# Kernel tuning notes

Measured on AMD Instinct MI355X. Metric: run time of the kernel, lower is better.

The kernel has to match this reference:

```python
import jax, jax.numpy as jnp
import numpy as np

N = 50000        # nodes
E = 800000       # edges (before self-loops)
IN = 512         # in_channels
HEADS = 8        # 'head' arg: heads and per-head out dim of conv1
C1 = 8           # per-head channels of conv1 (== head)
OUT = 128        # out_channels of conv2
NEG_SLOPE = 0.2  # PyG GATConv leaky-relu slope


def _glorot(key, shape, fan_in):
    return jax.random.normal(key, shape, jnp.float32) * (1.0 / np.sqrt(fan_in))


def setup_inputs() -> dict:
    key = jax.random.key(0)
    ks = jax.random.split(key, 10)
    x = jax.random.normal(ks[0], (N, IN), jnp.float32)
    edge_index = jax.random.randint(ks[1], (2, E), 0, N, dtype=jnp.int32)
    # conv1: GATConv(IN, C1, heads=HEADS, concat=True)
    W1 = _glorot(ks[2], (IN, HEADS * C1), IN)
    att_src1 = _glorot(ks[3], (HEADS, C1), C1)
    att_dst1 = _glorot(ks[4], (HEADS, C1), C1)
    bias1 = jnp.zeros((HEADS * C1,), jnp.float32)
    # conv2: GATConv(HEADS*C1, OUT, heads=1, concat=False)
    W2 = _glorot(ks[5], (HEADS * C1, OUT), HEADS * C1)
    att_src2 = _glorot(ks[6], (1, OUT), OUT)
    att_dst2 = _glorot(ks[7], (1, OUT), OUT)
    bias2 = jnp.zeros((OUT,), jnp.float32)
    return {"x": x, "edge_index": edge_index,
            "W1": W1, "att_src1": att_src1, "att_dst1": att_dst1, "bias1": bias1,
            "W2": W2, "att_src2": att_src2, "att_dst2": att_dst2, "bias2": bias2}


def gat_conv(x, src, dst, W, a_src, a_dst, bias, heads, concat):
    """PyG GATConv (eval mode, dropout off). src/dst already include self-loops."""
    n = x.shape[0]
    h = (x @ W).reshape(n, heads, -1)                 # [N, H, C]
    s = (h * a_src[None]).sum(-1)                     # [N, H] alpha_src per node
    d = (h * a_dst[None]).sum(-1)                     # [N, H] alpha_dst per node
    alpha = jax.nn.leaky_relu(s[src] + d[dst], NEG_SLOPE)  # [E, H]
    # segment softmax over incoming edges of each destination node
    amax = jax.ops.segment_max(alpha, dst, num_segments=n)  # [N, H]
    amax = jnp.where(jnp.isfinite(amax), amax, 0.0)
    ea = jnp.exp(alpha - amax[dst])                   # [E, H]
    denom = jax.ops.segment_sum(ea, dst, num_segments=n)
    w = ea / (denom[dst] + 1e-16)                     # [E, H]
    msg = h[src] * w[..., None]                       # [E, H, C]
    out = jax.ops.segment_sum(msg, dst, num_segments=n)  # [N, H, C]
    out = out.reshape(n, -1) if concat else out.mean(axis=1)
    return out + bias


def reference(x, edge_index, W1, att_src1, att_dst1, bias1,
              W2, att_src2, att_dst2, bias2):
    n = x.shape[0]
    loop = jnp.arange(n, dtype=edge_index.dtype)      # PyG adds self-loops
    src = jnp.concatenate([edge_index[0], loop])
    dst = jnp.concatenate([edge_index[1], loop])
    h = jax.nn.elu(gat_conv(x, src, dst, W1, att_src1, att_dst1, bias1,
                            heads=HEADS, concat=True))
    out = jax.nn.elu(gat_conv(h, src, dst, W2, att_src2, att_dst2, bias2,
                              heads=1, concat=False))
    return out
```

## Files before the change

### kernel.cpp

```cpp
#include <hip/hip_runtime.h>

#define NEG_SLOPE 0.2f

typedef __attribute__((ext_vector_type(8))) short bf16x8;
typedef __attribute__((ext_vector_type(4))) float f32x4;

__device__ __forceinline__ float leaky(float v) {
    return v > 0.0f ? v : NEG_SLOPE * v;
}
__device__ __forceinline__ float elu(float v) {
    return v > 0.0f ? v : (__expf(v) - 1.0f);
}
__device__ __forceinline__ short f2b(float f) {
    return (short)((__float_as_uint(f) + 0x8000u) >> 16);
}
__device__ __forceinline__ float bf2f(unsigned short v) {
    return __uint_as_float(((unsigned)v) << 16);
}

__global__ void prep_k(const float* __restrict__ W1, const float* __restrict__ W2,
                       unsigned short* __restrict__ w1s, unsigned short* __restrict__ w2s,
                       int* __restrict__ deg, int N) {
    int i = blockIdx.x * 256 + threadIdx.x;
    if (i < N) deg[i] = 0;
    if (i < 512 * 64) {
        int k = i >> 6, n = i & 63;
        int kt = k >> 5, kk = k & 31;
        int nt = n >> 4, nn = n & 15;
        int lane = (kk >> 3) * 16 + nn, j = kk & 7;
        w1s[(((size_t)(kt * 4 + nt)) * 64 + lane) * 8 + j] = (unsigned short)f2b(W1[i]);
    } else if (i < 512 * 64 + 64 * 128) {
        int i2 = i - 512 * 64;
        int k = i2 >> 7, n = i2 & 127;
        int kt = k >> 5, kk = k & 31;
        int nt = n >> 4, nn = n & 15;
        int lane = (kk >> 3) * 16 + nn, j = kk & 7;
        w2s[(((size_t)(kt * 8 + nt)) * 64 + lane) * 8 + j] = (unsigned short)f2b(W2[i2]);
    }
}

__global__ __launch_bounds__(256) void gemm1_k(const float* __restrict__ X,
                                               const unsigned short* __restrict__ Ws,
                                               const float* __restrict__ Asrc,
                                               const float* __restrict__ Adst,
                                               unsigned short* __restrict__ Hb,
                                               float* __restrict__ S,
                                               float* __restrict__ D, int N) {
    const int lane = threadIdx.x & 63;
    const int wave = threadIdx.x >> 6;
    const int m0 = blockIdx.x * 64 + wave * 16;
    const int q = lane >> 4, lc = lane & 15;
    const int arow = m0 + lc;
    const float* xrow = X + (size_t)min(arow, N - 1) * 512 + q * 8;
    const bf16x8* bW = (const bf16x8*)Ws;

    f32x4 acc[4] = {{0.f,0.f,0.f,0.f},{0.f,0.f,0.f,0.f},{0.f,0.f,0.f,0.f},{0.f,0.f,0.f,0.f}};

    for (int kt = 0; kt < 16; ++kt) {
        float4 a0 = *(const float4*)(xrow + kt * 32);
        float4 a1 = *(const float4*)(xrow + kt * 32 + 4);
        bf16x8 af;
        af[0] = f2b(a0.x); af[1] = f2b(a0.y); af[2] = f2b(a0.z); af[3] = f2b(a0.w);
        af[4] = f2b(a1.x); af[5] = f2b(a1.y); af[6] = f2b(a1.z); af[7] = f2b(a1.w);
#pragma unroll
        for (int nt = 0; nt < 4; ++nt) {
            bf16x8 bf = bW[(size_t)(kt * 4 + nt) * 64 + lane];
            acc[nt] = __builtin_amdgcn_mfma_f32_16x16x32_bf16(af, bf, acc[nt], 0, 0, 0);
        }
    }

    float asc[4], adc[4];
#pragma unroll
    for (int nt = 0; nt < 4; ++nt) { asc[nt] = Asrc[nt * 16 + lc]; adc[nt] = Adst[nt * 16 + lc]; }

#pragma unroll
    for (int r = 0; r < 4; ++r) {
        int row = m0 + q * 4 + r;
        bool ok = row < N;
        if (ok) {
#pragma unroll
            for (int nt = 0; nt < 4; ++nt)
                Hb[(size_t)row * 64 + nt * 16 + lc] = (unsigned short)f2b(acc[nt][r]);
        }
        float ps[4], pd[4];
#pragma unroll
        for (int nt = 0; nt < 4; ++nt) { ps[nt] = acc[nt][r] * asc[nt]; pd[nt] = acc[nt][r] * adc[nt]; }
#pragma unroll
        for (int off = 1; off < 8; off <<= 1) {
#pragma unroll
            for (int nt = 0; nt < 4; ++nt) {
                ps[nt] += __shfl_xor(ps[nt], off);
                pd[nt] += __shfl_xor(pd[nt], off);
            }
        }
        if (ok && !(lc & 7)) {
            int hb = lc >> 3;
#pragma unroll
            for (int nt = 0; nt < 4; ++nt) {
                S[(size_t)row * 8 + nt * 2 + hb] = ps[nt];
                D[(size_t)row * 8 + nt * 2 + hb] = pd[nt];
            }
        }
    }
}

__global__ __launch_bounds__(256) void gemm2_k(const unsigned short* __restrict__ X,
                                               const unsigned short* __restrict__ Ws,
                                               const float* __restrict__ Asrc,
                                               const float* __restrict__ Adst,
                                               unsigned short* __restrict__ Hb,
                                               float* __restrict__ S,
                                               float* __restrict__ D, int N) {
    const int lane = threadIdx.x & 63;
    const int wave = threadIdx.x >> 6;
    const int m0 = blockIdx.x * 64 + wave * 16;
    const int q = lane >> 4, lc = lane & 15;
    const int arow = m0 + lc;
    const unsigned short* xrow = X + (size_t)min(arow, N - 1) * 64 + q * 8;
    const bf16x8* bW = (const bf16x8*)Ws;

    f32x4 acc[8] = {{0.f,0.f,0.f,0.f},{0.f,0.f,0.f,0.f},{0.f,0.f,0.f,0.f},{0.f,0.f,0.f,0.f},
                    {0.f,0.f,0.f,0.f},{0.f,0.f,0.f,0.f},{0.f,0.f,0.f,0.f},{0.f,0.f,0.f,0.f}};

#pragma unroll
    for (int kt = 0; kt < 2; ++kt) {
        bf16x8 af = *(const bf16x8*)(xrow + kt * 32);
#pragma unroll
        for (int nt = 0; nt < 8; ++nt) {
            bf16x8 bf = bW[(size_t)(kt * 8 + nt) * 64 + lane];
            acc[nt] = __builtin_amdgcn_mfma_f32_16x16x32_bf16(af, bf, acc[nt], 0, 0, 0);
        }
    }

    float asc[8], adc[8];
#pragma unroll
    for (int nt = 0; nt < 8; ++nt) { asc[nt] = Asrc[nt * 16 + lc]; adc[nt] = Adst[nt * 16 + lc]; }

#pragma unroll
    for (int r = 0; r < 4; ++r) {
        int row = m0 + q * 4 + r;
        bool ok = row < N;
        if (ok) {
#pragma unroll
            for (int nt = 0; nt < 8; ++nt)
                Hb[(size_t)row * 128 + nt * 16 + lc] = (unsigned short)f2b(acc[nt][r]);
        }
        float ps = 0.f, pd = 0.f;
#pragma unroll
        for (int nt = 0; nt < 8; ++nt) { ps += acc[nt][r] * asc[nt]; pd += acc[nt][r] * adc[nt]; }
#pragma unroll
        for (int off = 1; off < 16; off <<= 1) {
            ps += __shfl_xor(ps, off);
            pd += __shfl_xor(pd, off);
        }
        if (ok && lc == 0) { S[row] = ps; D[row] = pd; }
    }
}

__global__ void deg_k(const int* __restrict__ dst, int E, int* __restrict__ deg) {
    int base = (blockIdx.x * blockDim.x + threadIdx.x) * 8;
    if (base + 8 <= E) {
        int4 a = *(const int4*)(dst + base);
        int4 b = *(const int4*)(dst + base + 4);
        atomicAdd(&deg[a.x], 1); atomicAdd(&deg[a.y], 1);
        atomicAdd(&deg[a.z], 1); atomicAdd(&deg[a.w], 1);
        atomicAdd(&deg[b.x], 1); atomicAdd(&deg[b.y], 1);
        atomicAdd(&deg[b.z], 1); atomicAdd(&deg[b.w], 1);
    } else {
        for (int e = base; e < E; ++e) atomicAdd(&deg[dst[e]], 1);
    }
}

__global__ __launch_bounds__(256) void scanA_k(const int* __restrict__ deg,
                                               int* __restrict__ rowptr,
                                               int* __restrict__ partials, int N) {
    __shared__ int s[256];
    const int t = threadIdx.x;
    const int base = blockIdx.x * 1024;
    int v[4];
    int idx = base + t * 4;
#pragma unroll
    for (int i = 0; i < 4; ++i) v[i] = (idx + i < N) ? deg[idx + i] + 1 : 0;
    int sum = v[0] + v[1] + v[2] + v[3];
    s[t] = sum;
    __syncthreads();
    for (int off = 1; off < 256; off <<= 1) {
        int x = (t >= off) ? s[t - off] : 0;
        __syncthreads();
        s[t] += x;
        __syncthreads();
    }
    int run = s[t] - sum;
#pragma unroll
    for (int i = 0; i < 4; ++i) {
        if (idx + i < N) rowptr[idx + i] = run;
        run += v[i];
    }
    if (t == 255) partials[blockIdx.x] = s[255];
}

__global__ __launch_bounds__(256) void scanB_k(const int* __restrict__ partials,
                                               int* __restrict__ poff,
                                               int* __restrict__ rowptr, int nb,
                                               int N, int Etot) {
    __shared__ int s[256];
    const int t = threadIdx.x;
    int v = (t < nb) ? partials[t] : 0;
    s[t] = v;
    __syncthreads();
    for (int off = 1; off < 256; off <<= 1) {
        int x = (t >= off) ? s[t - off] : 0;
        __syncthreads();
        s[t] += x;
        __syncthreads();
    }
    poff[t] = s[t] - v;
    if (t == 0) rowptr[N] = Etot;
}

__global__ void scanC_k(int* __restrict__ rowptr, const int* __restrict__ poff,
                        int* __restrict__ wp, int* __restrict__ srcs, int N) {
    int i = blockIdx.x * blockDim.x + threadIdx.x;
    if (i >= N) return;
    int r = rowptr[i] + poff[i >> 10];
    rowptr[i] = r;
    srcs[r] = i;
    wp[i] = r + 1;
}

__global__ void scatter_k(const int* __restrict__ ei, int E,
                          int* __restrict__ wp, int* __restrict__ srcs) {
    int base = (blockIdx.x * blockDim.x + threadIdx.x) * 4;
    if (base + 4 <= E) {
        int4 s = *(const int4*)(ei + base);
        int4 d = *(const int4*)(ei + E + base);
        int p0 = atomicAdd(&wp[d.x], 1);
        int p1 = atomicAdd(&wp[d.y], 1);
        int p2 = atomicAdd(&wp[d.z], 1);
        int p3 = atomicAdd(&wp[d.w], 1);
        srcs[p0] = s.x; srcs[p1] = s.y; srcs[p2] = s.z; srcs[p3] = s.w;
    } else {
        for (int e = base; e < E; ++e) {
            int p = atomicAdd(&wp[ei[E + e]], 1);
            srcs[p] = ei[e];
        }
    }
}

__global__ __launch_bounds__(256) void agg1_csr_k(const int* __restrict__ rowptr,
                                                  const int* __restrict__ srcs,
                                                  const float* __restrict__ S,
                                                  const float* __restrict__ D,
                                                  const unsigned short* __restrict__ Hb,
                                                  const float* __restrict__ bias,
                                                  unsigned short* __restrict__ out, int N) {
    const int wid = (blockIdx.x * 256 + threadIdx.x) >> 6;
    const int lane = threadIdx.x & 63;
    if (wid >= N) return;
    const int beg = rowptr[wid], end = rowptr[wid + 1];
    const int h = lane & 7;
    const int el = lane >> 3;
    const float dvh = D[(size_t)wid * 8 + h];

    float m = -1e30f;
    for (int i = beg + el; i < end; i += 8)
        m = fmaxf(m, leaky(S[(size_t)srcs[i] * 8 + h] + dvh));
#pragma unroll
    for (int off = 8; off < 64; off <<= 1)
        m = fmaxf(m, __shfl_xor(m, off));

    float acc = 0.0f, den = 0.0f;
    for (int base = beg; base < end; base += 8) {
        int i = base + el;
        int src_l = 0; float w_l = 0.0f;
        if (i < end) {
            src_l = srcs[i];
            w_l = __expf(leaky(S[(size_t)src_l * 8 + h] + dvh) - m);
        }
        den += w_l;
#pragma unroll
        for (int j = 0; j < 8; ++j) {
            float w = __shfl(w_l, j * 8 + (lane >> 3));
            int src = __builtin_amdgcn_readfirstlane(__shfl(src_l, j * 8));
            acc += w * bf2f(Hb[(size_t)src * 64 + lane]);
        }
    }
#pragma unroll
    for (int off = 8; off < 64; off <<= 1)
        den += __shfl_xor(den, off);
    float rden = 1.0f / (__shfl(den, lane >> 3) + 1e-16f);
    out[(size_t)wid * 64 + lane] = (unsigned short)f2b(elu(acc * rden + bias[lane]));
}

__global__ __launch_bounds__(256) void agg2_csr_k(const int* __restrict__ rowptr,
                                                  const int* __restrict__ srcs,
                                                  const float* __restrict__ S,
                                                  const float* __restrict__ D,
                                                  const unsigned short* __restrict__ Hb,
                                                  const float* __restrict__ bias,
                                                  float* __restrict__ out, int N) {
    const int wid = (blockIdx.x * 256 + threadIdx.x) >> 6;
    const int lane = threadIdx.x & 63;
    if (wid >= N) return;
    const int beg = rowptr[wid], end = rowptr[wid + 1];
    const float dvh = D[wid];
    const int c0 = lane * 2;

    float m = -1e30f;
    for (int i = beg + lane; i < end; i += 64)
        m = fmaxf(m, leaky(S[srcs[i]] + dvh));
#pragma unroll
    for (int off = 1; off < 64; off <<= 1)
        m = fmaxf(m, __shfl_xor(m, off));

    float acc0 = 0.0f, acc1 = 0.0f, den = 0.0f;
    for (int base = beg; base < end; base += 64) {
        int i = base + lane;
        int src_l = 0; float w_l = 0.0f;
        if (i < end) {
            src_l = srcs[i];
            w_l = __expf(leaky(S[src_l] + dvh) - m);
        }
        den += w_l;
        const int cnt = min(64, end - base);
        for (int j0 = 0; j0 < cnt; j0 += 8) {
#pragma unroll
            for (int u = 0; u < 8; ++u) {
                int j = j0 + u;
                float w = __shfl(w_l, j);
                int src = __builtin_amdgcn_readfirstlane(__shfl(src_l, j));
                unsigned p = *(const unsigned*)(Hb + (size_t)src * 128 + c0);
                acc0 += w * __uint_as_float(p << 16);
                acc1 += w * __uint_as_float(p & 0xffff0000u);
            }
        }
    }
#pragma unroll
    for (int off = 1; off < 64; off <<= 1)
        den += __shfl_xor(den, off);
    const float rden = 1.0f / (den + 1e-16f);
    float2 o;
    o.x = elu(acc0 * rden + bias[c0]);
    o.y = elu(acc1 * rden + bias[c0 + 1]);
    *(float2*)(out + (size_t)wid * 128 + c0) = o;
}

extern "C" void kernel_launch(void* const* d_in, const int* in_sizes, int n_in,
                              void* d_out, int out_size, void* d_ws, size_t ws_size,
                              hipStream_t stream) {
    const float* x   = (const float*)d_in[0];
    const int*   ei  = (const int*)d_in[1];
    const float* W1  = (const float*)d_in[2];
    const float* as1 = (const float*)d_in[3];
    const float* ad1 = (const float*)d_in[4];
    const float* b1  = (const float*)d_in[5];
    const float* W2  = (const float*)d_in[6];
    const float* as2 = (const float*)d_in[7];
    const float* ad2 = (const float*)d_in[8];
    const float* b2  = (const float*)d_in[9];

    const int N = in_sizes[0] / 512;
    const int E = in_sizes[1] / 2;
    const int Etot = E + N;
    float* out = (float*)d_out;

    unsigned short* w1s    = (unsigned short*)d_ws;
    unsigned short* w2s    = w1s + 512 * 64;
    unsigned short* out1b  = w2s + 64 * 128;
    unsigned short* h1b    = out1b + (size_t)N * 64;
    float*          s1     = (float*)(h1b + (size_t)N * 64);
    float*          d1     = s1 + (size_t)N * 8;
    unsigned short* h2b    = (unsigned short*)(d1 + (size_t)N * 8);
    float*          s2     = (float*)(h2b + (size_t)N * 128);
    float*          d2     = s2 + N;
    int*            rowptr = (int*)(d2 + N);
    int*            srcs   = rowptr + (N + 1);
    int* deg      = (int*)h2b;
    int* wp       = deg + N;
    int* partials = wp + N;
    int* poff     = partials + 256;

    const int B = 256;
    const int nb = (N + 1023) / 1024;
    const int gblk = (N + 63) / 64;
    const int prep_n = (N > 512 * 64 + 64 * 128) ? N : (512 * 64 + 64 * 128);

    prep_k<<<(prep_n + B - 1) / B, B, 0, stream>>>(W1, W2, w1s, w2s, deg, N);
    deg_k<<<(E + B * 8 - 1) / (B * 8), B, 0, stream>>>(ei + E, E, deg);
    scanA_k<<<nb, B, 0, stream>>>(deg, rowptr, partials, N);
    scanB_k<<<1, B, 0, stream>>>(partials, poff, rowptr, nb, N, Etot);
    scanC_k<<<(N + B - 1) / B, B, 0, stream>>>(rowptr, poff, wp, srcs, N);
    scatter_k<<<(E + B * 4 - 1) / (B * 4), B, 0, stream>>>(ei, E, wp, srcs);

    gemm1_k<<<gblk, B, 0, stream>>>(x, w1s, as1, ad1, h1b, s1, d1, N);
    agg1_csr_k<<<(N + 3) / 4, B, 0, stream>>>(rowptr, srcs, s1, d1, h1b, b1, out1b, N);

    gemm2_k<<<gblk, B, 0, stream>>>(out1b, w2s, as2, ad2, h2b, s2, d2, N);
    agg2_csr_k<<<(N + 3) / 4, B, 0, stream>>>(rowptr, srcs, s2, d2, h2b, b2, out, N);
}
```

Measured before the change: 364.8 us.

## Fuse degree count into GEMM1, single-pass ticket scan, fuse agg1 with GEMM2

Degree counting moves into extra blocks of the first GEMM launch, so the GEMM and the atomics run together in one kernel. The three-kernel scan becomes one kernel that takes each chunk's base offset from an atomic ticket counter, and row ends are rebuilt from beg+deg+1 instead of rowptr. The layer-1 aggregation now writes its bf16 results to shared memory and runs the second GEMM there, so out1b no longer goes through global memory. This removes several launches and one round trip through global memory. In exchange, ticket-ordered chunk bases make the CSR layout depend on block scheduling order, and agg1 waves now stall at a block barrier.

```diff
diff --git a/kernel.cpp b/kernel.cpp
--- a/kernel.cpp
+++ b/kernel.cpp
@@ -22,7 +22,7 @@
                        unsigned short* __restrict__ w1s, unsigned short* __restrict__ w2s,
                        int* __restrict__ deg, int N) {
     int i = blockIdx.x * 256 + threadIdx.x;
-    if (i < N) deg[i] = 0;
+    if (i <= N) deg[i] = 0;
     if (i < 512 * 64) {
         int k = i >> 6, n = i & 63;
         int kt = k >> 5, kk = k & 31;
@@ -39,13 +39,31 @@
     }
 }
 
-__global__ __launch_bounds__(256) void gemm1_k(const float* __restrict__ X,
+__global__ __launch_bounds__(256) void g1deg_k(const float* __restrict__ X,
                                                const unsigned short* __restrict__ Ws,
                                                const float* __restrict__ Asrc,
                                                const float* __restrict__ Adst,
                                                unsigned short* __restrict__ Hb,
                                                float* __restrict__ S,
-                                               float* __restrict__ D, int N) {
+                                               float* __restrict__ D,
+                                               const int* __restrict__ dst,
+                                               int* __restrict__ deg,
+                                               int N, int E, int gblk) {
+    if ((int)blockIdx.x >= gblk) {
+        int wtid = ((int)blockIdx.x - gblk) * 256 + threadIdx.x;
+        int base = wtid * 8;
+        if (base + 8 <= E) {
+            int4 a = *(const int4*)(dst + base);
+            int4 b = *(const int4*)(dst + base + 4);
+            atomicAdd(&deg[a.x], 1); atomicAdd(&deg[a.y], 1);
+            atomicAdd(&deg[a.z], 1); atomicAdd(&deg[a.w], 1);
+            atomicAdd(&deg[b.x], 1); atomicAdd(&deg[b.y], 1);
+            atomicAdd(&deg[b.z], 1); atomicAdd(&deg[b.w], 1);
+        } else {
+            for (int e = base; e < E; ++e) atomicAdd(&deg[dst[e]], 1);
+        }
+        return;
+    }
     const int lane = threadIdx.x & 63;
     const int wave = threadIdx.x >> 6;
     const int m0 = blockIdx.x * 64 + wave * 16;
@@ -104,128 +122,39 @@
     }
 }
 
-__global__ __launch_bounds__(256) void gemm2_k(const unsigned short* __restrict__ X,
-                                               const unsigned short* __restrict__ Ws,
-                                               const float* __restrict__ Asrc,
-                                               const float* __restrict__ Adst,
-                                               unsigned short* __restrict__ Hb,
-                                               float* __restrict__ S,
-                                               float* __restrict__ D, int N) {
-    const int lane = threadIdx.x & 63;
-    const int wave = threadIdx.x >> 6;
-    const int m0 = blockIdx.x * 64 + wave * 16;
-    const int q = lane >> 4, lc = lane & 15;
-    const int arow = m0 + lc;
-    const unsigned short* xrow = X + (size_t)min(arow, N - 1) * 64 + q * 8;
-    const bf16x8* bW = (const bf16x8*)Ws;
-
-    f32x4 acc[8] = {{0.f,0.f,0.f,0.f},{0.f,0.f,0.f,0.f},{0.f,0.f,0.f,0.f},{0.f,0.f,0.f,0.f},
-                    {0.f,0.f,0.f,0.f},{0.f,0.f,0.f,0.f},{0.f,0.f,0.f,0.f},{0.f,0.f,0.f,0.f}};
-
-#pragma unroll
-    for (int kt = 0; kt < 2; ++kt) {
-        bf16x8 af = *(const bf16x8*)(xrow + kt * 32);
-#pragma unroll
-        for (int nt = 0; nt < 8; ++nt) {
-            bf16x8 bf = bW[(size_t)(kt * 8 + nt) * 64 + lane];
-            acc[nt] = __builtin_amdgcn_mfma_f32_16x16x32_bf16(af, bf, acc[nt], 0, 0, 0);
-        }
-    }
-
-    float asc[8], adc[8];
-#pragma unroll
-    for (int nt = 0; nt < 8; ++nt) { asc[nt] = Asrc[nt * 16 + lc]; adc[nt] = Adst[nt * 16 + lc]; }
-
-#pragma unroll
-    for (int r = 0; r < 4; ++r) {
-        int row = m0 + q * 4 + r;
-        bool ok = row < N;
-        if (ok) {
-#pragma unroll
-            for (int nt = 0; nt < 8; ++nt)
-                Hb[(size_t)row * 128 + nt * 16 + lc] = (unsigned short)f2b(acc[nt][r]);
-        }
-        float ps = 0.f, pd = 0.f;
-#pragma unroll
-        for (int nt = 0; nt < 8; ++nt) { ps += acc[nt][r] * asc[nt]; pd += acc[nt][r] * adc[nt]; }
-#pragma unroll
-        for (int off = 1; off < 16; off <<= 1) {
-            ps += __shfl_xor(ps, off);
-            pd += __shfl_xor(pd, off);
-        }
-        if (ok && lc == 0) { S[row] = ps; D[row] = pd; }
-    }
-}
-
-__global__ void deg_k(const int* __restrict__ dst, int E, int* __restrict__ deg) {
-    int base = (blockIdx.x * blockDim.x + threadIdx.x) * 8;
-    if (base + 8 <= E) {
-        int4 a = *(const int4*)(dst + base);
-        int4 b = *(const int4*)(dst + base + 4);
-        atomicAdd(&deg[a.x], 1); atomicAdd(&deg[a.y], 1);
-        atomicAdd(&deg[a.z], 1); atomicAdd(&deg[a.w], 1);
-        atomicAdd(&deg[b.x], 1); atomicAdd(&deg[b.y], 1);
-        atomicAdd(&deg[b.z], 1); atomicAdd(&deg[b.w], 1);
-    } else {
-        for (int e = base; e < E; ++e) atomicAdd(&deg[dst[e]], 1);
-    }
-}
-
-__global__ __launch_bounds__(256) void scanA_k(const int* __restrict__ deg,
-                                               int* __restrict__ rowptr,
-                                               int* __restrict__ partials, int N) {
-    __shared__ int s[256];
+__global__ __launch_bounds__(256) void scan_k(const int* __restrict__ deg_in,
+                                              int* __restrict__ ticket,
+                                              int* __restrict__ beg,
+                                              int* __restrict__ wp,
+                                              int* __restrict__ srcs, int N) {
+    __shared__ int sm[256];
+    __shared__ int chunkBase;
     const int t = threadIdx.x;
-    const int base = blockIdx.x * 1024;
+    int idx = blockIdx.x * 1024 + t * 4;
     int v[4];
-    int idx = base + t * 4;
-#pragma unroll
-    for (int i = 0; i < 4; ++i) v[i] = (idx + i < N) ? deg[idx + i] + 1 : 0;
+#pragma unroll
+    for (int i = 0; i < 4; ++i) v[i] = (idx + i < N) ? deg_in[idx + i] + 1 : 0;
     int sum = v[0] + v[1] + v[2] + v[3];
-    s[t] = sum;
+    sm[t] = sum;
     __syncthreads();
     for (int off = 1; off < 256; off <<= 1) {
-        int x = (t >= off) ? s[t - off] : 0;
+        int xv = (t >= off) ? sm[t - off] : 0;
         __syncthreads();
-        s[t] += x;
+        sm[t] += xv;
         __syncthreads();
     }
-    int run = s[t] - sum;
+    if (t == 255) chunkBase = atomicAdd(ticket, sm[255]);
+    __syncthreads();
+    int run = chunkBase + sm[t] - sum;
 #pragma unroll
     for (int i = 0; i < 4; ++i) {
-        if (idx + i < N) rowptr[idx + i] = run;
-        run += v[i];
-    }
-    if (t == 255) partials[blockIdx.x] = s[255];
-}
-
-__global__ __launch_bounds__(256) void scanB_k(const int* __restrict__ partials,
-                                               int* __restrict__ poff,
-                                               int* __restrict__ rowptr, int nb,
-                                               int N, int Etot) {
-    __shared__ int s[256];
-    const int t = threadIdx.x;
-    int v = (t < nb) ? partials[t] : 0;
-    s[t] = v;
-    __syncthreads();
-    for (int off = 1; off < 256; off <<= 1) {
-        int x = (t >= off) ? s[t - off] : 0;
-        __syncthreads();
-        s[t] += x;
-        __syncthreads();
-    }
-    poff[t] = s[t] - v;
-    if (t == 0) rowptr[N] = Etot;
-}
-
-__global__ void scanC_k(int* __restrict__ rowptr, const int* __restrict__ poff,
-                        int* __restrict__ wp, int* __restrict__ srcs, int N) {
-    int i = blockIdx.x * blockDim.x + threadIdx.x;
-    if (i >= N) return;
-    int r = rowptr[i] + poff[i >> 10];
-    rowptr[i] = r;
-    srcs[r] = i;
-    wp[i] = r + 1;
+        if (idx + i < N) {
+            beg[idx + i] = run;
+            srcs[run] = idx + i;
+            wp[idx + i] = run + 1;
+            run += v[i];
+        }
+    }
 }
 
 __global__ void scatter_k(const int* __restrict__ ei, int E,
@@ -247,52 +176,124 @@
     }
 }
 
-__global__ __launch_bounds__(256) void agg1_csr_k(const int* __restrict__ rowptr,
-                                                  const int* __restrict__ srcs,
-                                                  const float* __restrict__ S,
-                                                  const float* __restrict__ D,
-                                                  const unsigned short* __restrict__ Hb,
-                                                  const float* __restrict__ bias,
-                                                  unsigned short* __restrict__ out, int N) {
-    const int wid = (blockIdx.x * 256 + threadIdx.x) >> 6;
-    const int lane = threadIdx.x & 63;
-    if (wid >= N) return;
-    const int beg = rowptr[wid], end = rowptr[wid + 1];
+__global__ __launch_bounds__(256) void agg1g2_k(const int* __restrict__ beg,
+                                                const int* __restrict__ deg,
+                                                const int* __restrict__ srcs,
+                                                const float* __restrict__ S1,
+                                                const float* __restrict__ D1,
+                                                const unsigned short* __restrict__ H1b,
+                                                const float* __restrict__ b1,
+                                                const unsigned short* __restrict__ W2s,
+                                                const float* __restrict__ as2,
+                                                const float* __restrict__ ad2,
+                                                unsigned short* __restrict__ H2b,
+                                                float* __restrict__ S2,
+                                                float* __restrict__ D2, int N) {
+    __shared__ unsigned short sh[16][64];
+    __shared__ float shp[4][16], shq[4][16];
+
+    const int tid  = threadIdx.x;
+    const int lane = tid & 63;
+    const int wave = tid >> 6;
+    const int m0 = blockIdx.x * 16;
+
     const int h = lane & 7;
     const int el = lane >> 3;
-    const float dvh = D[(size_t)wid * 8 + h];
-
-    float m = -1e30f;
-    for (int i = beg + el; i < end; i += 8)
-        m = fmaxf(m, leaky(S[(size_t)srcs[i] * 8 + h] + dvh));
-#pragma unroll
-    for (int off = 8; off < 64; off <<= 1)
-        m = fmaxf(m, __shfl_xor(m, off));
-
-    float acc = 0.0f, den = 0.0f;
-    for (int base = beg; base < end; base += 8) {
-        int i = base + el;
-        int src_l = 0; float w_l = 0.0f;
-        if (i < end) {
-            src_l = srcs[i];
-            w_l = __expf(leaky(S[(size_t)src_l * 8 + h] + dvh) - m);
-        }
-        den += w_l;
-#pragma unroll
-        for (int j = 0; j < 8; ++j) {
-            float w = __shfl(w_l, j * 8 + (lane >> 3));
-            int src = __builtin_amdgcn_readfirstlane(__shfl(src_l, j * 8));
-            acc += w * bf2f(Hb[(size_t)src * 64 + lane]);
-        }
-    }
-#pragma unroll
-    for (int off = 8; off < 64; off <<= 1)
-        den += __shfl_xor(den, off);
-    float rden = 1.0f / (__shfl(den, lane >> 3) + 1e-16f);
-    out[(size_t)wid * 64 + lane] = (unsigned short)f2b(elu(acc * rden + bias[lane]));
-}
-
-__global__ __launch_bounds__(256) void agg2_csr_k(const int* __restrict__ rowptr,
+#pragma unroll
+    for (int rep = 0; rep < 4; ++rep) {
+        const int nl = wave * 4 + rep;
+        const int wid = m0 + nl;
+        if (wid < N) {
+            const int b0 = beg[wid];
+            const int e0 = b0 + deg[wid] + 1;
+            const float dvh = D1[(size_t)wid * 8 + h];
+
+            float m = -1e30f;
+            for (int i = b0 + el; i < e0; i += 8)
+                m = fmaxf(m, leaky(S1[(size_t)srcs[i] * 8 + h] + dvh));
+#pragma unroll
+            for (int off = 8; off < 64; off <<= 1)
+                m = fmaxf(m, __shfl_xor(m, off));
+
+            float acc = 0.0f, den = 0.0f;
+            for (int base = b0; base < e0; base += 8) {
+                int i = base + el;
+                int src_l = 0; float w_l = 0.0f;
+                if (i < e0) {
+                    src_l = srcs[i];
+                    w_l = __expf(leaky(S1[(size_t)src_l * 8 + h] + dvh) - m);
+                }
+                den += w_l;
+#pragma unroll
+                for (int j = 0; j < 8; ++j) {
+                    float w = __shfl(w_l, j * 8 + (lane >> 3));
+                    int src = __builtin_amdgcn_readfirstlane(__shfl(src_l, j * 8));
+                    acc += w * bf2f(H1b[(size_t)src * 64 + lane]);
+                }
+            }
+#pragma unroll
+            for (int off = 8; off < 64; off <<= 1)
+                den += __shfl_xor(den, off);
+            float rden = 1.0f / (__shfl(den, lane >> 3) + 1e-16f);
+            sh[nl][lane] = (unsigned short)f2b(elu(acc * rden + b1[lane]));
+        } else {
+            sh[nl][lane] = 0;
+        }
+    }
+    __syncthreads();
+
+    const int q = lane >> 4, lc = lane & 15;
+    const bf16x8* bW = (const bf16x8*)W2s;
+    const int nt0 = wave * 2;
+
+    f32x4 acc2[2] = {{0.f,0.f,0.f,0.f},{0.f,0.f,0.f,0.f}};
+#pragma unroll
+    for (int kt = 0; kt < 2; ++kt) {
+        bf16x8 af = *(const bf16x8*)(&sh[lc][q * 8 + kt * 32]);
+#pragma unroll
+        for (int u = 0; u < 2; ++u) {
+            bf16x8 bf = bW[(size_t)(kt * 8 + nt0 + u) * 64 + lane];
+            acc2[u] = __builtin_amdgcn_mfma_f32_16x16x32_bf16(af, bf, acc2[u], 0, 0, 0);
+        }
+    }
+    float asc[2], adc[2];
+#pragma unroll
+    for (int u = 0; u < 2; ++u) {
+        asc[u] = as2[(nt0 + u) * 16 + lc];
+        adc[u] = ad2[(nt0 + u) * 16 + lc];
+    }
+#pragma unroll
+    for (int r = 0; r < 4; ++r) {
+        int rl = q * 4 + r;
+        int row = m0 + rl;
+        if (row < N) {
+#pragma unroll
+            for (int u = 0; u < 2; ++u)
+                H2b[(size_t)row * 128 + (nt0 + u) * 16 + lc] = (unsigned short)f2b(acc2[u][r]);
+        }
+        float ps = acc2[0][r] * asc[0] + acc2[1][r] * asc[1];
+        float pd = acc2[0][r] * adc[0] + acc2[1][r] * adc[1];
+#pragma unroll
+        for (int off = 1; off < 16; off <<= 1) {
+            ps += __shfl_xor(ps, off);
+            pd += __shfl_xor(pd, off);
+        }
+        if (lc == 0) { shp[wave][rl] = ps; shq[wave][rl] = pd; }
+    }
+    __syncthreads();
+    if (tid < 16) {
+        int row = m0 + tid;
+        if (row < N) {
+            float s = shp[0][tid] + shp[1][tid] + shp[2][tid] + shp[3][tid];
+            float d = shq[0][tid] + shq[1][tid] + shq[2][tid] + shq[3][tid];
+            S2[row] = s;
+            D2[row] = d;
+        }
+    }
+}
+
+__global__ __launch_bounds__(256) void agg2_csr_k(const int* __restrict__ beg,
+                                                  const int* __restrict__ deg,
                                                   const int* __restrict__ srcs,
                                                   const float* __restrict__ S,
                                                   const float* __restrict__ D,
@@ -302,36 +303,37 @@
     const int wid = (blockIdx.x * 256 + threadIdx.x) >> 6;
     const int lane = threadIdx.x & 63;
     if (wid >= N) return;
-    const int beg = rowptr[wid], end = rowptr[wid + 1];
-    const float dvh = D[wid];
+    const int b0 = beg[wid];
+    const int e0 = b0 + deg[wid] + 1;
+    const float dv = D[wid];
     const int c0 = lane * 2;
 
     float m = -1e30f;
-    for (int i = beg + lane; i < end; i += 64)
-        m = fmaxf(m, leaky(S[srcs[i]] + dvh));
+    for (int i = b0 + lane; i < e0; i += 64)
+        m = fmaxf(m, leaky(S[srcs[i]] + dv));
 #pragma unroll
     for (int off = 1; off < 64; off <<= 1)
         m = fmaxf(m, __shfl_xor(m, off));
 
     float acc0 = 0.0f, acc1 = 0.0f, den = 0.0f;
-    for (int base = beg; base < end; base += 64) {
+    for (int base = b0; base < e0; base += 64) {
         int i = base + lane;
         int src_l = 0; float w_l = 0.0f;
-        if (i < end) {
+        if (i < e0) {
             src_l = srcs[i];
-            w_l = __expf(leaky(S[src_l] + dvh) - m);
+            w_l = __expf(leaky(S[src_l] + dv) - m);
         }
         den += w_l;
-        const int cnt = min(64, end - base);
+        const int cnt = min(64, e0 - base);
         for (int j0 = 0; j0 < cnt; j0 += 8) {
 #pragma unroll
             for (int u = 0; u < 8; ++u) {
                 int j = j0 + u;
                 float w = __shfl(w_l, j);
                 int src = __builtin_amdgcn_readfirstlane(__shfl(src_l, j));
-                unsigned p = *(const unsigned*)(Hb + (size_t)src * 128 + c0);
-                acc0 += w * __uint_as_float(p << 16);
-                acc1 += w * __uint_as_float(p & 0xffff0000u);
+                unsigned pv = *(const unsigned*)(Hb + (size_t)src * 128 + c0);
+                acc0 += w * __uint_as_float(pv << 16);
+                acc1 += w * __uint_as_float(pv & 0xffff0000u);
             }
         }
     }
@@ -361,40 +363,34 @@
 
     const int N = in_sizes[0] / 512;
     const int E = in_sizes[1] / 2;
-    const int Etot = E + N;
-    float* out = (float*)d_out;
-
-    unsigned short* w1s    = (unsigned short*)d_ws;
-    unsigned short* w2s    = w1s + 512 * 64;
-    unsigned short* out1b  = w2s + 64 * 128;
-    unsigned short* h1b    = out1b + (size_t)N * 64;
-    float*          s1     = (float*)(h1b + (size_t)N * 64);
-    float*          d1     = s1 + (size_t)N * 8;
-    unsigned short* h2b    = (unsigned short*)(d1 + (size_t)N * 8);
-    float*          s2     = (float*)(h2b + (size_t)N * 128);
-    float*          d2     = s2 + N;
-    int*            rowptr = (int*)(d2 + N);
-    int*            srcs   = rowptr + (N + 1);
-    int* deg      = (int*)h2b;
-    int* wp       = deg + N;
-    int* partials = wp + N;
-    int* poff     = partials + 256;
+
+    unsigned short* w1s  = (unsigned short*)d_ws;
+    unsigned short* w2s  = w1s + 512 * 64;
+    unsigned short* h1b  = w2s + 64 * 128;
+    unsigned short* h2b  = h1b + (size_t)N * 64;
+    float*          s1   = (float*)(h2b + (size_t)N * 128);
+    float*          d1   = s1 + (size_t)N * 8;
+    float*          s2   = d1 + (size_t)N * 8;
+    float*          d2   = s2 + N;
+    int*            beg  = (int*)(d2 + N);
+    int*            deg  = beg + N;
+    int*            wp   = deg + (N + 1);
+    int*            srcs = wp + N;
 
     const int B = 256;
-    const int nb = (N + 1023) / 1024;
     const int gblk = (N + 63) / 64;
-    const int prep_n = (N > 512 * 64 + 64 * 128) ? N : (512 * 64 + 64 * 128);
+    const int degb = (E / 8 + B - 1) / B;
+    const int nb   = (N + 1023) / 1024;
+    int prep_n = 512 * 64 + 64 * 128;
+    if (N + 1 > prep_n) prep_n = N + 1;
 
     prep_k<<<(prep_n + B - 1) / B, B, 0, stream>>>(W1, W2, w1s, w2s, deg, N);
-    deg_k<<<(E + B * 8 - 1) / (B * 8), B, 0, stream>>>(ei + E, E, deg);
-    scanA_k<<<nb, B, 0, stream>>>(deg, rowptr, partials, N);
-    scanB_k<<<1, B, 0, stream>>>(partials, poff, rowptr, nb, N, Etot);
-    scanC_k<<<(N + B - 1) / B, B, 0, stream>>>(rowptr, poff, wp, srcs, N);
+    g1deg_k<<<gblk + degb, B, 0, stream>>>(x, w1s, as1, ad1, h1b, s1, d1,
+                                           ei + E, deg, N, E, gblk);
+    scan_k<<<nb, B, 0, stream>>>(deg, deg + N, beg, wp, srcs, N);
     scatter_k<<<(E + B * 4 - 1) / (B * 4), B, 0, stream>>>(ei, E, wp, srcs);
-
-    gemm1_k<<<gblk, B, 0, stream>>>(x, w1s, as1, ad1, h1b, s1, d1, N);
-    agg1_csr_k<<<(N + 3) / 4, B, 0, stream>>>(rowptr, srcs, s1, d1, h1b, b1, out1b, N);
-
-    gemm2_k<<<gblk, B, 0, stream>>>(out1b, w2s, as2, ad2, h2b, s2, d2, N);
-    agg2_csr_k<<<(N + 3) / 4, B, 0, stream>>>(rowptr, srcs, s2, d2, h2b, b2, out, N);
-}
+    agg1g2_k<<<(N + 15) / 16, B, 0, stream>>>(beg, deg, srcs, s1, d1, h1b, b1,
+                                              w2s, as2, ad2, h2b, s2, d2, N);
+    agg2_csr_k<<<(N + 3) / 4, B, 0, stream>>>(beg, deg, srcs, s2, d2, h2b, b2,
+                                              (float*)d_out, N);
+}
```

Result: faster. 354.9 us (-2.7%).
